# Optimization experiments

Measured on AMD Instinct MI355X. Metric: run time of the kernel, lower is better.

## Reference

```python
import math
import jax, jax.numpy as jnp
import numpy as np


def _tokenformer_theta(scores):
    # L2-normalize along last dim, scale by sqrt(n), then exact GELU (torch F.gelu default)
    n = scores.shape[-1]
    l2 = jnp.maximum(jnp.linalg.norm(scores, ord=2, axis=-1, keepdims=True), 1e-8)
    scaled = scores * (math.sqrt(n) / l2)
    return jax.nn.gelu(scaled, approximate=False)


def setup_inputs() -> dict:
    key = jax.random.key(0)
    k1, k2, k3 = jax.random.split(key, 3)
    B, T, C = 4, 2048, 1024
    heads, num_tokens = 8, 1024
    key_hd, val_hd = C // heads, 1024 // heads
    x = jax.random.normal(k1, (B, T, C), dtype=jnp.float32)
    # kaiming_uniform_(a=sqrt(5)) on [heads, num_tokens, head_dim]: bound = sqrt(6/((1+5)*fan_in)) = 1/sqrt(fan_in)
    bk = 1.0 / math.sqrt(num_tokens)
    key_tokens = jax.random.uniform(k2, (heads, num_tokens, key_hd), minval=-bk, maxval=bk, dtype=jnp.float32)
    val_tokens = jax.random.uniform(k3, (heads, num_tokens, val_hd), minval=-bk, maxval=bk, dtype=jnp.float32)
    return {"x": x, "key_tokens": key_tokens, "val_tokens": val_tokens}


def reference(x, key_tokens, val_tokens):
    B, T, C = x.shape
    H, N, Dk = key_tokens.shape
    # q: [B, H, T, Dk]
    q = x.reshape(B, T, H, Dk).transpose(0, 2, 1, 3)
    # scores: [B, H, T, N]
    scores = jnp.einsum('bhtd,hnd->bhtn', q, key_tokens)
    scores = _tokenformer_theta(scores)
    # ThresHot: hard hot-mask keeping entries above the per-row mean (straight-through quantizer)
    mask = scores > jnp.mean(scores, axis=-1, keepdims=True)
    scores = jnp.where(mask, scores, 0.0)
    # out: [B, H, T, Dv] -> [B, T, H*Dv]
    out = jnp.einsum('bhtn,hnv->bhtv', scores, val_tokens)
    return out.transpose(0, 2, 1, 3).reshape(B, T, -1)
```

## Files before the change

### kernel.cpp

```cpp
#include <hip/hip_runtime.h>
#include <cstdint>
#include <cmath>


typedef __bf16 bf16x8 __attribute__((ext_vector_type(8)));
typedef float  f32x16 __attribute__((ext_vector_type(16)));
typedef unsigned short u16x8 __attribute__((ext_vector_type(8)));

__device__ __forceinline__ unsigned short f2bf(float f) {
  unsigned int u = __float_as_uint(f);
  unsigned int r = (u + 0x7FFFu + ((u >> 16) & 1u)) >> 16;
  return (unsigned short)r;
}
__device__ __forceinline__ float bf2f(unsigned short b) {
  return __uint_as_float(((unsigned int)b) << 16);
}

__device__ __forceinline__ float gelu_exact(float v) {
  const float s = v * 0.70710678118654752f;
  const float a = fabsf(s);
  const float t = __builtin_amdgcn_rcpf(fmaf(0.3275911f, a, 1.0f));
  float p = fmaf(1.061405429f, t, -1.453152027f);
  p = fmaf(p, t, 1.421413741f);
  p = fmaf(p, t, -0.284496736f);
  p = fmaf(p, t, 0.254829592f);
  p *= t;
  const float e = __expf(-a * a);
  float er = fmaf(-p, e, 1.0f);
  er = copysignf(er, s);
  return 0.5f * v * (1.0f + er);
}

__global__ void prep_k(const float* __restrict__ key,
                       unsigned short* __restrict__ kh,
                       unsigned short* __restrict__ kl) {
  const int tid = blockIdx.x * 256 + threadIdx.x;
  const int h   = tid >> 14;
  const int s2  = (tid >> 10) & 15;
  const int n   = tid & 1023;
  const float* src = key + ((size_t)(h << 10) + n) * 128 + s2 * 8;
  const float4 f0 = *(const float4*)src;
  const float4 f1 = *(const float4*)(src + 4);
  const float fv[8] = {f0.x, f0.y, f0.z, f0.w, f1.x, f1.y, f1.z, f1.w};
  u16x8 hv, lv;
#pragma unroll
  for (int e = 0; e < 8; ++e) {
    const unsigned short hb = f2bf(fv[e]);
    hv[e] = hb;
    lv[e] = f2bf(fv[e] - bf2f(hb));
  }
  const size_t o = ((size_t)(h * 16 + s2) * 1024 + n) * 8;
  *(u16x8*)(kh + o) = hv;
  *(u16x8*)(kl + o) = lv;
}

__global__ void prep_v(const float* __restrict__ val,
                       unsigned short* __restrict__ vp) {
  const int tid = blockIdx.x * 256 + threadIdx.x;
  const int h   = tid >> 14;
  const int s2  = (tid >> 7) & 127;
  const int v   = tid & 127;
  const float* src = val + ((size_t)(h << 10) + s2 * 8) * 128 + v;
  u16x8 ov;
#pragma unroll
  for (int e = 0; e < 8; ++e) ov[e] = f2bf(src[(size_t)e * 128]);
  *(u16x8*)(vp + ((size_t)(h * 128 + s2) * 128 + v) * 8) = ov;
}

#define RED1   65536
#define RED2   66560
#define SMEMSZ 67584

__global__ __launch_bounds__(512, 4) void fused_mhk(
    const float* __restrict__ x,
    const unsigned short* __restrict__ k_hi,
    const unsigned short* __restrict__ k_lo,
    const unsigned short* __restrict__ v_pk,
    float* __restrict__ out)
{
  extern __shared__ char smem[];
  const int tid  = threadIdx.x;
  const int wave = tid >> 6;
  const int lane = tid & 63;
  const int l31  = lane & 31;
  const int hi   = lane >> 5;

  const int bid = blockIdx.x;
  const int h   = bid & 7;
  const int b   = (bid >> 3) & 3;
  const int tt  = bid >> 5;
  const int t0  = tt * 32;

  {
    const float* xq = x + ((size_t)(b * 2048 + t0)) * 1024 + h * 128;
    const int r  = tid >> 4;
    const int ci = tid & 15;
    const float* sp = xq + (size_t)r * 1024 + ci * 8;
    const float4 f0 = *(const float4*)sp;
    const float4 f1 = *(const float4*)(sp + 4);
    const float fv[8] = {f0.x, f0.y, f0.z, f0.w, f1.x, f1.y, f1.z, f1.w};
    u16x8 hv, lv;
#pragma unroll
    for (int e = 0; e < 8; ++e) {
      const unsigned short hb = f2bf(fv[e]);
      hv[e] = hb;
      lv[e] = f2bf(fv[e] - bf2f(hb));
    }
    const int cb = (ci * 16) ^ ((r & 15) << 4);
    *(u16x8*)(smem + r * 256 + cb) = hv;
    *(u16x8*)(smem + 8192 + r * 256 + cb) = lv;
  }
  __syncthreads();

  f32x16 acc[4];
#pragma unroll
  for (int t = 0; t < 4; ++t)
#pragma unroll
    for (int i = 0; i < 16; ++i) acc[t][i] = 0.f;

  {
    const unsigned short* khh = k_hi + (size_t)h * 131072;
    const unsigned short* khl = k_lo + (size_t)h * 131072;
    const int qoff = (l31 & 15) << 4;
#pragma unroll
    for (int s = 0; s < 8; ++s) {
      const int cb = ((32 * s + 16 * hi) ^ qoff) + l31 * 256;
      const bf16x8 bqh = *(const bf16x8*)(smem + cb);
      const bf16x8 bql = *(const bf16x8*)(smem + 8192 + cb);
      const size_t kbase = (size_t)(s * 2 + hi) * 8192 +
                           (size_t)(wave * 128 + l31) * 8;
#pragma unroll
      for (int t = 0; t < 4; ++t) {
        const bf16x8 ah = *(const bf16x8*)(khh + kbase + t * 256);
        const bf16x8 al = *(const bf16x8*)(khl + kbase + t * 256);
        acc[t] = __builtin_amdgcn_mfma_f32_32x32x16_bf16(ah, bqh, acc[t], 0, 0, 0);
        acc[t] = __builtin_amdgcn_mfma_f32_32x32x16_bf16(ah, bql, acc[t], 0, 0, 0);
        acc[t] = __builtin_amdgcn_mfma_f32_32x32x16_bf16(al, bqh, acc[t], 0, 0, 0);
      }
    }
  }

  float* red1 = (float*)(smem + RED1);
  float* red2 = (float*)(smem + RED2);

  float ss = 0.f;
#pragma unroll
  for (int t = 0; t < 4; ++t)
#pragma unroll
    for (int i = 0; i < 16; ++i) ss += acc[t][i] * acc[t][i];
  ss += __shfl_xor(ss, 32);
  if (lane < 32) red1[wave * 32 + lane] = ss;
  __syncthreads();
  float sum = 0.f;
#pragma unroll
  for (int w = 0; w < 8; ++w) sum += red1[w * 32 + l31];
  const float scale = 32.0f / fmaxf(sqrtf(sum), 1e-8f);

  float gs = 0.f;
#pragma unroll
  for (int t = 0; t < 4; ++t)
#pragma unroll
    for (int i = 0; i < 16; ++i) {
      const float g = gelu_exact(acc[t][i] * scale);
      acc[t][i] = g;
      gs += g;
    }
  gs += __shfl_xor(gs, 32);
  if (lane < 32) red2[wave * 32 + lane] = gs;
  __syncthreads();
  float mean = 0.f;
#pragma unroll
  for (int w = 0; w < 8; ++w) mean += red2[w * 32 + l31];
  mean *= (1.0f / 1024.0f);

  {
    const int swz  = (l31 & 31) << 4;
    const int rowb = l31 * 2048;
#pragma unroll
    for (int t = 0; t < 4; ++t) {
#pragma unroll
      for (int g = 0; g < 4; ++g) {
        float g0 = acc[t][4 * g + 0]; g0 = (g0 > mean) ? g0 : 0.f;
        float g1 = acc[t][4 * g + 1]; g1 = (g1 > mean) ? g1 : 0.f;
        float g2 = acc[t][4 * g + 2]; g2 = (g2 > mean) ? g2 : 0.f;
        float g3 = acc[t][4 * g + 3]; g3 = (g3 > mean) ? g3 : 0.f;
        const unsigned int u0 = (unsigned)f2bf(g0) | ((unsigned)f2bf(g1) << 16);
        const unsigned int u1 = (unsigned)f2bf(g2) | ((unsigned)f2bf(g3) << 16);
        const int cb = (wave * 256 + t * 64 + 8 * hi + 16 * g) ^ swz;
        *(uint2*)(smem + rowb + cb) = make_uint2(u0, u1);
      }
    }
  }
  __syncthreads();

  if (wave >= 4) return;
  const int vt = wave;
  f32x16 o;
#pragma unroll
  for (int i = 0; i < 16; ++i) o[i] = 0.f;

  const unsigned short* vp = v_pk + (size_t)h * 131072 + (size_t)hi * 1024 +
                             (size_t)(vt * 32 + l31) * 8;
  const int swz  = (l31 & 31) << 4;
  const int rowb = l31 * 2048;
#pragma unroll 8
  for (int s = 0; s < 64; ++s) {
    const bf16x8 aa = *(const bf16x8*)(smem + rowb + ((32 * s + 16 * hi) ^ swz));
    const bf16x8 bb = *(const bf16x8*)(vp + (size_t)s * 2048);
    o = __builtin_amdgcn_mfma_f32_32x32x16_bf16(aa, bb, o, 0, 0, 0);
  }

  float* op = out + ((size_t)(b * 2048 + t0)) * 1024 + h * 128 + vt * 32 + l31;
#pragma unroll
  for (int r = 0; r < 16; ++r) {
    const int q = (r & 3) + 8 * (r >> 2) + 4 * hi;
    op[(size_t)q * 1024] = o[r];
  }
}


extern "C" void kernel_launch(void* const* d_in, const int* in_sizes, int n_in,
                              void* d_out, int out_size, void* d_ws, size_t ws_size,
                              hipStream_t stream) {
  const float* x   = (const float*)d_in[0];
  const float* key = (const float*)d_in[1];
  const float* val = (const float*)d_in[2];
  float* out = (float*)d_out;

  if (ws_size < (size_t)6 * 1024 * 1024) return;

  unsigned short* k_hi = (unsigned short*)d_ws;
  unsigned short* k_lo = k_hi + 1048576;
  unsigned short* v_pk = k_lo + 1048576;

  prep_k<<<dim3(512), dim3(256), 0, stream>>>(key, k_hi, k_lo);
  prep_v<<<dim3(512), dim3(256), 0, stream>>>(val, v_pk);
  fused_mhk<<<dim3(2048), dim3(512), SMEMSZ, stream>>>(x, k_hi, k_lo, v_pk, out);
}
```

Before: 111.9 us.

## Process 64 tokens per block and reuse K tiles across two query tiles

Each block now covers 64 tokens with 1024 threads. Every K fragment loaded from global memory feeds MFMAs for two 32-token query tiles, which halves the K hi/lo traffic per token. The second GEMM is rewritten with 16x16x32 MFMAs so all 16 waves take part, where previously half the waves exited early. The LDS layout and swizzles are redone, and manual bf16 rounding is replaced with native __bf16 casts. The cost is about 136KB of LDS per block, which limits residency to one block per CU and adds larger block-wide barriers.

```diff
diff --git a/kernel.cpp b/kernel.cpp
--- a/kernel.cpp
+++ b/kernel.cpp
@@ -5,15 +5,11 @@
 
 typedef __bf16 bf16x8 __attribute__((ext_vector_type(8)));
 typedef float  f32x16 __attribute__((ext_vector_type(16)));
+typedef float  f32x4  __attribute__((ext_vector_type(4)));
 typedef unsigned short u16x8 __attribute__((ext_vector_type(8)));
 
-__device__ __forceinline__ unsigned short f2bf(float f) {
-  unsigned int u = __float_as_uint(f);
-  unsigned int r = (u + 0x7FFFu + ((u >> 16) & 1u)) >> 16;
-  return (unsigned short)r;
-}
-__device__ __forceinline__ float bf2f(unsigned short b) {
-  return __uint_as_float(((unsigned int)b) << 16);
+__device__ __forceinline__ unsigned short bfbits(__bf16 b) {
+  return __builtin_bit_cast(unsigned short, b);
 }
 
 __device__ __forceinline__ float gelu_exact(float v) {
@@ -36,20 +32,20 @@
                        unsigned short* __restrict__ kl) {
   const int tid = blockIdx.x * 256 + threadIdx.x;
   const int h   = tid >> 14;
-  const int s2  = (tid >> 10) & 15;
+  const int kc  = (tid >> 10) & 15;
   const int n   = tid & 1023;
-  const float* src = key + ((size_t)(h << 10) + n) * 128 + s2 * 8;
+  const float* src = key + ((size_t)(h << 10) + n) * 128 + kc * 8;
   const float4 f0 = *(const float4*)src;
   const float4 f1 = *(const float4*)(src + 4);
   const float fv[8] = {f0.x, f0.y, f0.z, f0.w, f1.x, f1.y, f1.z, f1.w};
   u16x8 hv, lv;
 #pragma unroll
   for (int e = 0; e < 8; ++e) {
-    const unsigned short hb = f2bf(fv[e]);
-    hv[e] = hb;
-    lv[e] = f2bf(fv[e] - bf2f(hb));
-  }
-  const size_t o = ((size_t)(h * 16 + s2) * 1024 + n) * 8;
+    const __bf16 hb = (__bf16)fv[e];
+    hv[e] = bfbits(hb);
+    lv[e] = bfbits((__bf16)(fv[e] - (float)hb));
+  }
+  const size_t o = ((size_t)(h * 16 + kc) * 1024 + n) * 8;
   *(u16x8*)(kh + o) = hv;
   *(u16x8*)(kl + o) = lv;
 }
@@ -63,15 +59,15 @@
   const float* src = val + ((size_t)(h << 10) + s2 * 8) * 128 + v;
   u16x8 ov;
 #pragma unroll
-  for (int e = 0; e < 8; ++e) ov[e] = f2bf(src[(size_t)e * 128]);
+  for (int e = 0; e < 8; ++e) ov[e] = bfbits((__bf16)src[(size_t)e * 128]);
   *(u16x8*)(vp + ((size_t)(h * 128 + s2) * 128 + v) * 8) = ov;
 }
 
-#define RED1   65536
-#define RED2   66560
-#define SMEMSZ 67584
-
-__global__ __launch_bounds__(512, 4) void fused_mhk(
+#define RED1   131072
+#define RED2   135168
+#define SMEMSZ 139264
+
+__global__ __launch_bounds__(1024, 4) void fused_mhk(
     const float* __restrict__ x,
     const unsigned short* __restrict__ k_hi,
     const unsigned short* __restrict__ k_lo,
@@ -87,55 +83,66 @@
 
   const int bid = blockIdx.x;
   const int h   = bid & 7;
-  const int b   = (bid >> 3) & 3;
-  const int tt  = bid >> 5;
-  const int t0  = tt * 32;
+  const int g8  = bid >> 3;
+  const int b   = g8 & 3;
+  const int tt  = g8 >> 2;
+  const int t0  = tt * 64;
 
   {
     const float* xq = x + ((size_t)(b * 2048 + t0)) * 1024 + h * 128;
     const int r  = tid >> 4;
-    const int ci = tid & 15;
-    const float* sp = xq + (size_t)r * 1024 + ci * 8;
+    const int kc = tid & 15;
+    const float* sp = xq + (size_t)r * 1024 + kc * 8;
     const float4 f0 = *(const float4*)sp;
     const float4 f1 = *(const float4*)(sp + 4);
     const float fv[8] = {f0.x, f0.y, f0.z, f0.w, f1.x, f1.y, f1.z, f1.w};
-    u16x8 hv, lv;
+    bf16x8 hv; u16x8 lv;
 #pragma unroll
     for (int e = 0; e < 8; ++e) {
-      const unsigned short hb = f2bf(fv[e]);
+      const __bf16 hb = (__bf16)fv[e];
       hv[e] = hb;
-      lv[e] = f2bf(fv[e] - bf2f(hb));
-    }
-    const int cb = (ci * 16) ^ ((r & 15) << 4);
-    *(u16x8*)(smem + r * 256 + cb) = hv;
-    *(u16x8*)(smem + 8192 + r * 256 + cb) = lv;
-  }
-  __syncthreads();
-
-  f32x16 acc[4];
-#pragma unroll
-  for (int t = 0; t < 4; ++t)
-#pragma unroll
-    for (int i = 0; i < 16; ++i) acc[t][i] = 0.f;
+      lv[e] = bfbits((__bf16)(fv[e] - (float)hb));
+    }
+    const int g = kc * 64 + (r ^ ((kc >> 1) & 7));
+    *(bf16x8*)(smem + g * 16) = hv;
+    *(u16x8*)(smem + 16384 + g * 16) = lv;
+  }
+  __syncthreads();
+
+  f32x16 acc[2][2];
+#pragma unroll
+  for (int t = 0; t < 2; ++t)
+#pragma unroll
+    for (int qt = 0; qt < 2; ++qt)
+#pragma unroll
+      for (int i = 0; i < 16; ++i) acc[t][qt][i] = 0.f;
 
   {
-    const unsigned short* khh = k_hi + (size_t)h * 131072;
-    const unsigned short* khl = k_lo + (size_t)h * 131072;
-    const int qoff = (l31 & 15) << 4;
+    const unsigned short* kph = k_hi + (size_t)h * 131072;
+    const unsigned short* kpl = k_lo + (size_t)h * 131072;
+    const size_t kb = (size_t)hi * 8192 + (size_t)(wave * 64 + l31) * 8;
+    const int hi64 = hi * 64;
 #pragma unroll
     for (int s = 0; s < 8; ++s) {
-      const int cb = ((32 * s + 16 * hi) ^ qoff) + l31 * 256;
-      const bf16x8 bqh = *(const bf16x8*)(smem + cb);
-      const bf16x8 bql = *(const bf16x8*)(smem + 8192 + cb);
-      const size_t kbase = (size_t)(s * 2 + hi) * 8192 +
-                           (size_t)(wave * 128 + l31) * 8;
-#pragma unroll
-      for (int t = 0; t < 4; ++t) {
-        const bf16x8 ah = *(const bf16x8*)(khh + kbase + t * 256);
-        const bf16x8 al = *(const bf16x8*)(khl + kbase + t * 256);
-        acc[t] = __builtin_amdgcn_mfma_f32_32x32x16_bf16(ah, bqh, acc[t], 0, 0, 0);
-        acc[t] = __builtin_amdgcn_mfma_f32_32x32x16_bf16(ah, bql, acc[t], 0, 0, 0);
-        acc[t] = __builtin_amdgcn_mfma_f32_32x32x16_bf16(al, bqh, acc[t], 0, 0, 0);
+      bf16x8 bqh[2], bql[2];
+#pragma unroll
+      for (int qt = 0; qt < 2; ++qt) {
+        const int gx = (2 * s) * 64 + hi64 + ((qt * 32 + l31) ^ s);
+        bqh[qt] = *(const bf16x8*)(smem + gx * 16);
+        bql[qt] = *(const bf16x8*)(smem + 16384 + gx * 16);
+      }
+      const unsigned short* kah = kph + kb + s * 16384;
+      const unsigned short* kal = kpl + kb + s * 16384;
+#pragma unroll
+      for (int t = 0; t < 2; ++t) {
+        const bf16x8 ah = *(const bf16x8*)(kah + t * 256);
+        const bf16x8 al = *(const bf16x8*)(kal + t * 256);
+        acc[t][0] = __builtin_amdgcn_mfma_f32_32x32x16_bf16(ah, bqh[0], acc[t][0], 0, 0, 0);
+        acc[t][1] = __builtin_amdgcn_mfma_f32_32x32x16_bf16(ah, bqh[1], acc[t][1], 0, 0, 0);
+        acc[t][0] = __builtin_amdgcn_mfma_f32_32x32x16_bf16(ah, bql[0], acc[t][0], 0, 0, 0);
+        acc[t][1] = __builtin_amdgcn_mfma_f32_32x32x16_bf16(ah, bql[1], acc[t][1], 0, 0, 0);
+        acc[t][0] = __builtin_amdgcn_mfma_f32_32x32x16_bf16(al, bqh[0], acc[t][0], 0, 0, 0);
+        acc[t][1] = __builtin_amdgcn_mfma_f32_32x32x16_bf16(al, bqh[1], acc[t][1], 0, 0, 0);
       }
     }
   }
@@ -143,78 +150,108 @@
   float* red1 = (float*)(smem + RED1);
   float* red2 = (float*)(smem + RED2);
 
-  float ss = 0.f;
-#pragma unroll
-  for (int t = 0; t < 4; ++t)
-#pragma unroll
-    for (int i = 0; i < 16; ++i) ss += acc[t][i] * acc[t][i];
-  ss += __shfl_xor(ss, 32);
-  if (lane < 32) red1[wave * 32 + lane] = ss;
-  __syncthreads();
-  float sum = 0.f;
-#pragma unroll
-  for (int w = 0; w < 8; ++w) sum += red1[w * 32 + l31];
-  const float scale = 32.0f / fmaxf(sqrtf(sum), 1e-8f);
-
-  float gs = 0.f;
-#pragma unroll
-  for (int t = 0; t < 4; ++t)
+  float ss0 = 0.f, ss1 = 0.f;
+#pragma unroll
+  for (int t = 0; t < 2; ++t)
 #pragma unroll
     for (int i = 0; i < 16; ++i) {
-      const float g = gelu_exact(acc[t][i] * scale);
-      acc[t][i] = g;
-      gs += g;
-    }
-  gs += __shfl_xor(gs, 32);
-  if (lane < 32) red2[wave * 32 + lane] = gs;
-  __syncthreads();
-  float mean = 0.f;
-#pragma unroll
-  for (int w = 0; w < 8; ++w) mean += red2[w * 32 + l31];
-  mean *= (1.0f / 1024.0f);
-
-  {
-    const int swz  = (l31 & 31) << 4;
-    const int rowb = l31 * 2048;
-#pragma unroll
-    for (int t = 0; t < 4; ++t) {
-#pragma unroll
-      for (int g = 0; g < 4; ++g) {
-        float g0 = acc[t][4 * g + 0]; g0 = (g0 > mean) ? g0 : 0.f;
-        float g1 = acc[t][4 * g + 1]; g1 = (g1 > mean) ? g1 : 0.f;
-        float g2 = acc[t][4 * g + 2]; g2 = (g2 > mean) ? g2 : 0.f;
-        float g3 = acc[t][4 * g + 3]; g3 = (g3 > mean) ? g3 : 0.f;
-        const unsigned int u0 = (unsigned)f2bf(g0) | ((unsigned)f2bf(g1) << 16);
-        const unsigned int u1 = (unsigned)f2bf(g2) | ((unsigned)f2bf(g3) << 16);
-        const int cb = (wave * 256 + t * 64 + 8 * hi + 16 * g) ^ swz;
-        *(uint2*)(smem + rowb + cb) = make_uint2(u0, u1);
+      ss0 += acc[t][0][i] * acc[t][0][i];
+      ss1 += acc[t][1][i] * acc[t][1][i];
+    }
+  ss0 += __shfl_xor(ss0, 32);
+  ss1 += __shfl_xor(ss1, 32);
+  if (lane < 32) {
+    red1[wave * 64 + lane]      = ss0;
+    red1[wave * 64 + 32 + lane] = ss1;
+  }
+  __syncthreads();
+  float sum0 = 0.f, sum1 = 0.f;
+#pragma unroll
+  for (int w = 0; w < 16; ++w) {
+    sum0 += red1[w * 64 + l31];
+    sum1 += red1[w * 64 + 32 + l31];
+  }
+  const float scale0 = 32.0f / fmaxf(sqrtf(sum0), 1e-8f);
+  const float scale1 = 32.0f / fmaxf(sqrtf(sum1), 1e-8f);
+
+  float gs0 = 0.f, gs1 = 0.f;
+#pragma unroll
+  for (int t = 0; t < 2; ++t)
+#pragma unroll
+    for (int i = 0; i < 16; ++i) {
+      const float g0 = gelu_exact(acc[t][0][i] * scale0);
+      acc[t][0][i] = g0; gs0 += g0;
+      const float g1 = gelu_exact(acc[t][1][i] * scale1);
+      acc[t][1][i] = g1; gs1 += g1;
+    }
+  gs0 += __shfl_xor(gs0, 32);
+  gs1 += __shfl_xor(gs1, 32);
+  if (lane < 32) {
+    red2[wave * 64 + lane]      = gs0;
+    red2[wave * 64 + 32 + lane] = gs1;
+  }
+  __syncthreads();
+  float mean0 = 0.f, mean1 = 0.f;
+#pragma unroll
+  for (int w = 0; w < 16; ++w) {
+    mean0 += red2[w * 64 + l31];
+    mean1 += red2[w * 64 + 32 + l31];
+  }
+  mean0 *= (1.0f / 1024.0f);
+  mean1 *= (1.0f / 1024.0f);
+
+#pragma unroll
+  for (int t = 0; t < 2; ++t) {
+#pragma unroll
+    for (int qt = 0; qt < 2; ++qt) {
+      const float mn = qt ? mean1 : mean0;
+      const int q = qt * 32 + l31;
+#pragma unroll
+      for (int gi = 0; gi < 4; ++gi) {
+        float g0 = acc[t][qt][4 * gi + 0]; g0 = (g0 > mn) ? g0 : 0.f;
+        float g1 = acc[t][qt][4 * gi + 1]; g1 = (g1 > mn) ? g1 : 0.f;
+        float g2 = acc[t][qt][4 * gi + 2]; g2 = (g2 > mn) ? g2 : 0.f;
+        float g3 = acc[t][qt][4 * gi + 3]; g3 = (g3 > mn) ? g3 : 0.f;
+        uint2 pk;
+        pk.x = (unsigned)bfbits((__bf16)g0) | ((unsigned)bfbits((__bf16)g1) << 16);
+        pk.y = (unsigned)bfbits((__bf16)g2) | ((unsigned)bfbits((__bf16)g3) << 16);
+        const int ng = wave * 8 + t * 4 + gi;
+        const int swz = (t * 4 + gi) & 7;
+        *(uint2*)(smem + (ng * 64 + (q ^ swz)) * 16 + hi * 8) = pk;
       }
     }
   }
   __syncthreads();
 
-  if (wave >= 4) return;
-  const int vt = wave;
-  f32x16 o;
-#pragma unroll
-  for (int i = 0; i < 16; ++i) o[i] = 0.f;
-
-  const unsigned short* vp = v_pk + (size_t)h * 131072 + (size_t)hi * 1024 +
-                             (size_t)(vt * 32 + l31) * 8;
-  const int swz  = (l31 & 31) << 4;
-  const int rowb = l31 * 2048;
+  const int l15 = lane & 15;
+  const int l4  = lane >> 4;
+  const int qt2 = wave >> 3;
+  const int vt  = wave & 7;
+
+  f32x4 o0, o1;
+#pragma unroll
+  for (int i = 0; i < 4; ++i) { o0[i] = 0.f; o1[i] = 0.f; }
+
+  const unsigned short* vb = v_pk + (size_t)h * 131072 + (size_t)l4 * 1024 +
+                             (size_t)(vt * 16 + l15) * 8;
+  const int qa = qt2 * 32 + l15;
 #pragma unroll 8
-  for (int s = 0; s < 64; ++s) {
-    const bf16x8 aa = *(const bf16x8*)(smem + rowb + ((32 * s + 16 * hi) ^ swz));
-    const bf16x8 bb = *(const bf16x8*)(vp + (size_t)s * 2048);
-    o = __builtin_amdgcn_mfma_f32_32x32x16_bf16(aa, bb, o, 0, 0, 0);
-  }
-
-  float* op = out + ((size_t)(b * 2048 + t0)) * 1024 + h * 128 + vt * 32 + l31;
-#pragma unroll
-  for (int r = 0; r < 16; ++r) {
-    const int q = (r & 3) + 8 * (r >> 2) + 4 * hi;
-    op[(size_t)q * 1024] = o[r];
+  for (int ks = 0; ks < 32; ++ks) {
+    const int swz = (ks & 1) * 4 + l4;
+    const int ngb = (ks * 4 + l4) * 64;
+    const bf16x8 a0 = *(const bf16x8*)(smem + (ngb + (qa ^ swz)) * 16);
+    const bf16x8 a1 = *(const bf16x8*)(smem + (ngb + ((qa + 16) ^ swz)) * 16);
+    const bf16x8 bb = *(const bf16x8*)(vb + (size_t)ks * 4096);
+    o0 = __builtin_amdgcn_mfma_f32_16x16x32_bf16(a0, bb, o0, 0, 0, 0);
+    o1 = __builtin_amdgcn_mfma_f32_16x16x32_bf16(a1, bb, o1, 0, 0, 0);
+  }
+
+  float* op = out + ((size_t)(b * 2048 + t0 + qt2 * 32 + l4 * 4)) * 1024 +
+              h * 128 + vt * 16 + l15;
+#pragma unroll
+  for (int j = 0; j < 4; ++j) {
+    op[(size_t)j * 1024]        = o0[j];
+    op[(size_t)(16 + j) * 1024] = o1[j];
   }
 }
 
@@ -235,5 +272,5 @@
 
   prep_k<<<dim3(512), dim3(256), 0, stream>>>(key, k_hi, k_lo);
   prep_v<<<dim3(512), dim3(256), 0, stream>>>(val, v_pk);
-  fused_mhk<<<dim3(2048), dim3(512), SMEMSZ, stream>>>(x, k_hi, k_lo, v_pk, out);
-}
+  fused_mhk<<<dim3(1024), dim3(1024), SMEMSZ, stream>>>(x, k_hi, k_lo, v_pk, out);
+}
```

After: 113.7 us. No clear change (+1.6%).
